# Kernel optimization log

Hardware: AMD Instinct MI355X
Metric: run time of the kernel (lower is better)

Reference implementation:

```python
import jax, jax.numpy as jnp
import numpy as np

HIDDEN = 1024
HEADS = 16
HEAD_DIM = HIDDEN // HEADS
B, S = 2, 2048


def setup_inputs() -> dict:
    key = jax.random.key(0)
    ks = jax.random.split(key, 11)
    std = 1.0 / np.sqrt(HIDDEN)
    return {
        "query": jax.random.normal(ks[0], (B, S, HIDDEN), dtype=jnp.float32),
        "key": jax.random.normal(ks[1], (B, S, HIDDEN), dtype=jnp.float32),
        "value": jax.random.normal(ks[2], (B, S, HIDDEN), dtype=jnp.float32),
        "Wq": jax.random.uniform(ks[3], (HIDDEN, HIDDEN), jnp.float32, -std, std),
        "bq": jax.random.uniform(ks[4], (HIDDEN,), jnp.float32, -std, std),
        "Wk": jax.random.uniform(ks[5], (HIDDEN, HIDDEN), jnp.float32, -std, std),
        "bk": jax.random.uniform(ks[6], (HIDDEN,), jnp.float32, -std, std),
        "Wv": jax.random.uniform(ks[7], (HIDDEN, HIDDEN), jnp.float32, -std, std),
        "bv": jax.random.uniform(ks[8], (HIDDEN,), jnp.float32, -std, std),
        "Wo": jax.random.uniform(ks[9], (HIDDEN, HIDDEN), jnp.float32, -std, std),
        "bo": jax.random.uniform(ks[10], (HIDDEN,), jnp.float32, -std, std),
    }


def reference(query, key, value, Wq, bq, Wk, bk, Wv, bv, Wo, bo):
    b = query.shape[0]
    scale = jnp.sqrt(jnp.float32(HEAD_DIM))
    # linear projections (torch Linear: x @ W.T + b), split into heads -> [b, h, s, d]
    def proj(x, W, bias):
        y = x @ W.T + bias
        return y.reshape(b, -1, HEADS, HEAD_DIM).transpose(0, 2, 1, 3)
    Q = proj(query, Wq, bq)
    K = proj(key, Wk, bk)
    V = proj(value, Wv, bv)
    scores = jnp.einsum("bhqd,bhkd->bhqk", Q, K) / scale
    attn = jax.nn.softmax(scores, axis=-1)
    ctx = jnp.einsum("bhqk,bhkd->bhqd", attn, V)
    ctx = ctx.transpose(0, 2, 1, 3).reshape(b, -1, HIDDEN)
    return ctx @ Wo.T + bo
```

## Files before the change

### kernel.cpp

```cpp
#include <hip/hip_runtime.h>

typedef __attribute__((ext_vector_type(8))) short short8;
typedef __attribute__((ext_vector_type(4))) float float4_t;
typedef __attribute__((ext_vector_type(4))) unsigned int uint4_t;
typedef __attribute__((ext_vector_type(2))) unsigned int uint2_t;
typedef unsigned short u16;

#define HIDDEN 1024
#define HDIM   64
#define SS     2048
#define TOK    4096
#define QSCALE 0.1803368801111137f

__device__ __forceinline__ unsigned int fbits(float f) {
  unsigned int x; __builtin_memcpy(&x, &f, 4); return x;
}
__device__ __forceinline__ u16 f2bf(float f) {
  return (u16)((fbits(f) + 0x8000u) >> 16);
}
__device__ __forceinline__ unsigned int pk2bf(float a, float b) {
  return __builtin_amdgcn_perm(fbits(b) + 0x8000u, fbits(a) + 0x8000u, 0x07060302);
}
__device__ __forceinline__ unsigned int pk2bf_t(float a, float b) {
  return __builtin_amdgcn_perm(fbits(b), fbits(a), 0x07060302);
}

__device__ __forceinline__ void gl_lds16(const u16* g, u16* l) {
  __builtin_amdgcn_global_load_lds(
      (const __attribute__((address_space(1))) unsigned int*)g,
      (__attribute__((address_space(3))) unsigned int*)l, 16, 0, 0);
}

__global__ __launch_bounds__(256) void convert_all(
    const float* __restrict__ w0, const float* __restrict__ w1,
    const float* __restrict__ w2, const float* __restrict__ w3,
    const float* __restrict__ x0, const float* __restrict__ x1,
    const float* __restrict__ x2, u16* __restrict__ Wall, u16* __restrict__ Xall) {
  int y = blockIdx.y;
  const float* src; u16* dst;
  if (y < 4) {
    if (blockIdx.x >= 512) return;
    src = y == 0 ? w0 : y == 1 ? w1 : y == 2 ? w2 : w3;
    dst = Wall + ((size_t)y << 20);
  } else {
    src = y == 4 ? x0 : y == 5 ? x1 : x2;
    dst = Xall + ((size_t)(y - 4) << 22);
  }
  int g = (blockIdx.x * 256 + threadIdx.x) * 8;
  float4_t a = *(const float4_t*)(src + g);
  float4_t b = *(const float4_t*)(src + g + 4);
  uint4_t o;
  o.x = pk2bf(a[0], a[1]); o.y = pk2bf(a[2], a[3]);
  o.z = pk2bf(b[0], b[1]); o.w = pk2bf(b[2], b[3]);
  *(uint4_t*)(dst + g) = o;
}

template<int MTILES, bool AXF32, bool OUTF32>
__device__ __forceinline__ void gemm_bt_body(
    const void* __restrict__ X, const u16* __restrict__ Wb,
    const float* __restrict__ bias, void* __restrict__ Y, int mode, float oscale,
    u16* sA, u16* sB, int row0, int col0) {
  const int tid  = threadIdx.x;
  const int wv   = tid >> 6, lane = tid & 63, quad = lane >> 4, ln = lane & 15;
  const int wm   = (wv >> 1) * (MTILES * 16), wn = (wv & 1) * 64;
  constexpr int AITERS = MTILES;

  float4_t acc[MTILES][4];
#pragma unroll
  for (int i = 0; i < MTILES; i++)
#pragma unroll
    for (int j = 0; j < 4; j++) acc[i][j] = (float4_t)0.0f;

  for (int kt = 0; kt < 16; ++kt) {
    const int k0 = kt * 64;
    short8 ax[AITERS];
    if (AXF32) {
#pragma unroll
      for (int i = 0; i < AITERS; i++) {
        int idx = i * 256 + tid, r = idx >> 3, c = idx & 7;
        const float* p = (const float*)X + (size_t)(row0 + r) * HIDDEN + k0 + c * 8;
        float4_t a = *(const float4_t*)p;
        float4_t b = *(const float4_t*)(p + 4);
        union { unsigned int u[4]; short8 s; } x;
        x.u[0] = pk2bf(a[0], a[1]); x.u[1] = pk2bf(a[2], a[3]);
        x.u[2] = pk2bf(b[0], b[1]); x.u[3] = pk2bf(b[2], b[3]);
        ax[i] = x.s;
      }
    }
    __syncthreads();
#pragma unroll
    for (int i = 0; i < 4; i++) {
      int idx = i * 256 + tid, r = idx >> 3, c = idx & 7;
      int gc = c ^ (r & 7);
      gl_lds16(Wb + (size_t)(col0 + r) * HIDDEN + k0 + gc * 8, sB + idx * 8);
    }
    if (AXF32) {
#pragma unroll
      for (int i = 0; i < AITERS; i++) {
        int idx = i * 256 + tid, r = idx >> 3, c = idx & 7;
        int pos = c ^ (r & 7);
        *(short8*)(sA + r * 64 + pos * 8) = ax[i];
      }
    } else {
#pragma unroll
      for (int i = 0; i < AITERS; i++) {
        int idx = i * 256 + tid, r = idx >> 3, c = idx & 7;
        int gc = c ^ (r & 7);
        gl_lds16((const u16*)X + (size_t)(row0 + r) * HIDDEN + k0 + gc * 8, sA + idx * 8);
      }
    }
    __syncthreads();

    short8 af[MTILES][2], bfr[4][2];
#pragma unroll
    for (int mt = 0; mt < MTILES; mt++)
#pragma unroll
      for (int kk = 0; kk < 2; kk++) {
        int r = wm + mt * 16 + ln;
        int ch = kk * 4 + quad;
        af[mt][kk] = *(const short8*)(sA + r * 64 + (ch ^ (r & 7)) * 8);
      }
#pragma unroll
    for (int nt = 0; nt < 4; nt++)
#pragma unroll
      for (int kk = 0; kk < 2; kk++) {
        int r = wn + nt * 16 + ln;
        int ch = kk * 4 + quad;
        bfr[nt][kk] = *(const short8*)(sB + r * 64 + (ch ^ (r & 7)) * 8);
      }
#pragma unroll
    for (int kk = 0; kk < 2; kk++)
#pragma unroll
      for (int mt = 0; mt < MTILES; mt++)
#pragma unroll
        for (int nt = 0; nt < 4; nt++)
          acc[mt][nt] = __builtin_amdgcn_mfma_f32_16x16x32_bf16(af[mt][kk], bfr[nt][kk], acc[mt][nt], 0, 0, 0);
  }

  float bcol[4];
#pragma unroll
  for (int nt = 0; nt < 4; nt++) bcol[nt] = bias[col0 + wn + nt * 16 + ln];
#pragma unroll
  for (int mt = 0; mt < MTILES; mt++)
#pragma unroll
    for (int nt = 0; nt < 4; nt++) {
      int n = col0 + wn + nt * 16 + ln;
#pragma unroll
      for (int r = 0; r < 4; r++) {
        int m = row0 + wm + mt * 16 + quad * 4 + r;
        float v = (acc[mt][nt][r] + bcol[nt]) * oscale;
        if (mode == 0) {
          if (OUTF32) ((float*)Y)[(size_t)m * HIDDEN + n] = v;
          else        ((u16*)Y)[(size_t)m * HIDDEN + n] = f2bf(v);
        } else {
          ((u16*)Y)[((size_t)(m >> 11) * HIDDEN + n) * SS + (m & 2047)] = f2bf(v);
        }
      }
    }
}

__global__ __launch_bounds__(256) void qkv_gemm_bf16(
    const u16* __restrict__ Xall, const u16* __restrict__ Wall,
    const float* __restrict__ bq, const float* __restrict__ bk, const float* __restrict__ bv,
    u16* __restrict__ Qp, u16* __restrict__ Kp, u16* __restrict__ Vt) {
  __shared__ u16 sA[128 * 64];
  __shared__ u16 sB[128 * 64];
  int z = blockIdx.z;
  const u16* X = Xall + ((size_t)z << 22);
  const u16* W = Wall + ((size_t)z << 20);
  const float* Bp = z == 0 ? bq : z == 1 ? bk : bv;
  u16* Y = z == 0 ? Qp : z == 1 ? Kp : Vt;
  int mode = (z == 2) ? 1 : 0;
  float sc = (z == 0) ? QSCALE : 1.0f;
  gemm_bt_body<4, false, false>(X, W, Bp, Y, mode, sc, sA, sB, blockIdx.y * 128, blockIdx.x * 128);
}

__global__ __launch_bounds__(256) void qkv_gemm_f32(
    const float* __restrict__ xq, const float* __restrict__ xk, const float* __restrict__ xv,
    const u16* __restrict__ Wall,
    const float* __restrict__ bq, const float* __restrict__ bk, const float* __restrict__ bv,
    u16* __restrict__ Qp, u16* __restrict__ Kp, u16* __restrict__ Vt) {
  __shared__ u16 sA[128 * 64];
  __shared__ u16 sB[128 * 64];
  int z = blockIdx.z;
  const float* X = z == 0 ? xq : z == 1 ? xk : xv;
  const u16* W = Wall + ((size_t)z << 20);
  const float* Bp = z == 0 ? bq : z == 1 ? bk : bv;
  u16* Y = z == 0 ? Qp : z == 1 ? Kp : Vt;
  int mode = (z == 2) ? 1 : 0;
  float sc = (z == 0) ? QSCALE : 1.0f;
  gemm_bt_body<4, true, false>(X, W, Bp, Y, mode, sc, sA, sB, blockIdx.y * 128, blockIdx.x * 128);
}

__global__ __launch_bounds__(256) void out_gemm(
    const u16* __restrict__ X, const u16* __restrict__ Wob,
    const float* __restrict__ bias, float* __restrict__ Y) {
  __shared__ u16 sA[64 * 64];
  __shared__ u16 sB[128 * 64];
  gemm_bt_body<2, false, true>(X, Wob, bias, Y, 0, 1.0f, sA, sB, blockIdx.y * 64, blockIdx.x * 128);
}

__global__ __launch_bounds__(256) void attn(
    const u16* __restrict__ Qp, const u16* __restrict__ Kp,
    const u16* __restrict__ Vt, u16* __restrict__ Ctx) {
  __shared__ u16 sK[128 * 64];
  __shared__ u16 sV[80 * 128];
  __shared__ u16 sP[4 * 32 * 64];
  const int tid  = threadIdx.x;
  const int wv   = tid >> 6, lane = tid & 63, quad = lane >> 4, ln = lane & 15;
  const int qt = blockIdx.x, h = blockIdx.y, b = blockIdx.z;
  const int row0 = qt * 128 + wv * 32;

  {
    int rr = 64 + (tid >> 4), cc = (tid & 15) * 8;
    short8 vv;
#pragma unroll
    for (int j = 0; j < 8; j++) vv[j] = (rr == 64) ? (short)0x3F80 : (short)0;
    *(short8*)(sV + rr * 128 + cc) = vv;
  }

  short8 qf[2][2];
#pragma unroll
  for (int j = 0; j < 2; j++)
#pragma unroll
    for (int kk = 0; kk < 2; kk++)
      qf[j][kk] = *(const short8*)(Qp + (size_t)(b * SS + row0 + j * 16 + ln) * HIDDEN
                                   + h * HDIM + kk * 32 + quad * 8);

  float4_t oacc[2][5];
#pragma unroll
  for (int j = 0; j < 2; j++)
#pragma unroll
    for (int t = 0; t < 5; t++) oacc[j][t] = (float4_t)0.f;

  u16* myP = sP + wv * 32 * 64;

  for (int kt = 0; kt < 16; ++kt) {
    __syncthreads();
#pragma unroll
    for (int p = 0; p < 4; p++) {
      int off = p * 256 + tid;
      { int r = off >> 3, c = off & 7;  int gc = c ^ (r & 7);
        gl_lds16(Kp + (size_t)(b * SS + kt * 128 + r) * HIDDEN + h * HDIM + gc * 8, sK + off * 8); }
      { int r = off >> 4, c = off & 15; int gc = c ^ (r & 15);
        gl_lds16(Vt + ((size_t)b * HIDDEN + h * HDIM + r) * SS + kt * 128 + gc * 8, sV + off * 8); }
    }
    __syncthreads();

#pragma unroll
    for (int half = 0; half < 2; half++) {
      float4_t st[4][2];
#pragma unroll
      for (int nt4 = 0; nt4 < 4; nt4++) {
        int nt = half * 4 + nt4;
#pragma unroll
        for (int j = 0; j < 2; j++) st[nt4][j] = (float4_t)0.f;
#pragma unroll
        for (int kk = 0; kk < 2; kk++) {
          int r = nt * 16 + ln;
          int ch = kk * 4 + quad;
          short8 kfr = *(const short8*)(sK + r * 64 + (ch ^ (r & 7)) * 8);
#pragma unroll
          for (int j = 0; j < 2; j++)
            st[nt4][j] = __builtin_amdgcn_mfma_f32_16x16x32_bf16(kfr, qf[j][kk], st[nt4][j], 0, 0, 0);
        }
      }

#pragma unroll
      for (int nt4 = 0; nt4 < 4; nt4++)
#pragma unroll
        for (int j = 0; j < 2; j++) {
          float p0 = __builtin_amdgcn_exp2f(fminf(st[nt4][j][0], 80.f));
          float p1 = __builtin_amdgcn_exp2f(fminf(st[nt4][j][1], 80.f));
          float p2 = __builtin_amdgcn_exp2f(fminf(st[nt4][j][2], 80.f));
          float p3 = __builtin_amdgcn_exp2f(fminf(st[nt4][j][3], 80.f));
          uint2_t w; w.x = pk2bf_t(p0, p1); w.y = pk2bf_t(p2, p3);
          int row = j * 16 + ln;
          int c2 = nt4 * 2 + (quad >> 1);
          int pos = c2 ^ (row & 7);
          *(uint2_t*)(myP + row * 64 + pos * 8 + (quad & 1) * 4) = w;
        }

#pragma unroll
      for (int ks = 0; ks < 2; ks++) {
        int CH = half * 8 + ks * 4 + quad;
        short8 vf[5];
#pragma unroll
        for (int dt = 0; dt < 5; dt++) {
          int d = dt * 16 + ln;
          vf[dt] = *(const short8*)(sV + d * 128 + ((CH ^ (d & 15))) * 8);
        }
#pragma unroll
        for (int j = 0; j < 2; j++) {
          int row = j * 16 + ln;
          int c2 = ks * 4 + quad;
          short8 pb = *(const short8*)(myP + row * 64 + (c2 ^ (row & 7)) * 8);
#pragma unroll
          for (int dt = 0; dt < 5; dt++)
            oacc[j][dt] = __builtin_amdgcn_mfma_f32_16x16x32_bf16(vf[dt], pb, oacc[j][dt], 0, 0, 0);
        }
      }
    }
  }

#pragma unroll
  for (int j = 0; j < 2; j++) {
    float inv = 1.0f / __shfl(oacc[j][4][0], ln, 64);
#pragma unroll
    for (int dt = 0; dt < 4; dt++) {
      uint2_t w;
      w.x = pk2bf(oacc[j][dt][0] * inv, oacc[j][dt][1] * inv);
      w.y = pk2bf(oacc[j][dt][2] * inv, oacc[j][dt][3] * inv);
      int row = j * 16 + ln;
      int ch = dt * 2 + (quad >> 1);
      int pos = ch ^ (row & 7);
      *(uint2_t*)(myP + row * 64 + pos * 8 + (quad & 1) * 4) = w;
    }
  }
#pragma unroll
  for (int jr = 0; jr < 2; jr++)
#pragma unroll
    for (int jc = 0; jc < 2; jc++) {
      int q = lane >> 2;
      int row = jr * 16 + q;
      int c = jc * 4 + (lane & 3);
      int pos = c ^ (row & 7);
      short8 o8 = *(const short8*)(myP + row * 64 + pos * 8);
      *(short8*)(Ctx + (size_t)(b * SS + row0 + row) * HIDDEN + h * HDIM + c * 8) = o8;
    }
}

extern "C" void kernel_launch(void* const* d_in, const int* in_sizes, int n_in,
                              void* d_out, int out_size, void* d_ws, size_t ws_size,
                              hipStream_t stream) {
  const float* q  = (const float*)d_in[0];
  const float* k  = (const float*)d_in[1];
  const float* v  = (const float*)d_in[2];
  const float* Wq = (const float*)d_in[3];
  const float* bq = (const float*)d_in[4];
  const float* Wk = (const float*)d_in[5];
  const float* bk = (const float*)d_in[6];
  const float* Wv = (const float*)d_in[7];
  const float* bv = (const float*)d_in[8];
  const float* Wo = (const float*)d_in[9];
  const float* bo = (const float*)d_in[10];

  u16* Qp   = (u16*)d_ws;
  u16* Kp   = Qp + (size_t)TOK * HIDDEN;
  u16* Vt   = Kp + (size_t)TOK * HIDDEN;
  u16* Wall = Vt + (size_t)TOK * HIDDEN;
  u16* Xall = Wall + (4u << 20);
  u16* Cx   = Qp;
  bool useX = ws_size >= (size_t)56 * 1024 * 1024;

  dim3 blk(256);
  if (useX) {
    hipLaunchKernelGGL(convert_all, dim3(2048, 7), blk, 0, stream,
                       Wq, Wk, Wv, Wo, q, k, v, Wall, Xall);
    hipLaunchKernelGGL(qkv_gemm_bf16, dim3(8, 32, 3), blk, 0, stream,
                       Xall, Wall, bq, bk, bv, Qp, Kp, Vt);
  } else {
    hipLaunchKernelGGL(convert_all, dim3(512, 4), blk, 0, stream,
                       Wq, Wk, Wv, Wo, q, k, v, Wall, Wall);
    hipLaunchKernelGGL(qkv_gemm_f32, dim3(8, 32, 3), blk, 0, stream,
                       q, k, v, Wall, bq, bk, bv, Qp, Kp, Vt);
  }
  hipLaunchKernelGGL(attn, dim3(16, 16, 2), blk, 0, stream, Qp, Kp, Vt, Cx);
  hipLaunchKernelGGL(out_gemm, dim3(8, 64, 1), blk, 0, stream,
                     Cx, Wall + (3u << 20), bo, (float*)d_out);
}
```

Baseline: 236.0 us.

## Rewrite attention with 32x32 MFMA, register-resident P, and double-buffered K/V

The attention kernel moves from 16x16x32 to 32x32x16 bf16 MFMA, with each wave covering 64 query rows. Softmax probabilities are repacked in registers via permlane32_swap, so the LDS round trip for P goes away. The row sum is accumulated in registers, which drops the extra ones-row MFMA tile. K/V tiles are double-buffered so loading the next tile overlaps compute, the grid becomes a flat 256 blocks (one per CU), and launch bounds are set to one block per SM. The trade-off is higher register pressure and lower occupancy, plus a grid that relies on a fixed 256-CU mapping.

```diff
diff --git a/kernel.cpp b/kernel.cpp
--- a/kernel.cpp
+++ b/kernel.cpp
@@ -2,6 +2,7 @@
 
 typedef __attribute__((ext_vector_type(8))) short short8;
 typedef __attribute__((ext_vector_type(4))) float float4_t;
+typedef __attribute__((ext_vector_type(16))) float f32x16;
 typedef __attribute__((ext_vector_type(4))) unsigned int uint4_t;
 typedef __attribute__((ext_vector_type(2))) unsigned int uint2_t;
 typedef unsigned short u16;
@@ -200,134 +201,135 @@
   gemm_bt_body<2, false, true>(X, Wob, bias, Y, 0, 1.0f, sA, sB, blockIdx.y * 64, blockIdx.x * 128);
 }
 
-__global__ __launch_bounds__(256) void attn(
+__global__ __launch_bounds__(256, 1) void attn(
     const u16* __restrict__ Qp, const u16* __restrict__ Kp,
     const u16* __restrict__ Vt, u16* __restrict__ Ctx) {
-  __shared__ u16 sK[128 * 64];
-  __shared__ u16 sV[80 * 128];
-  __shared__ u16 sP[4 * 32 * 64];
+  __shared__ u16 sK[2][128 * 64];
+  __shared__ u16 sV[2][64 * 128];
   const int tid  = threadIdx.x;
-  const int wv   = tid >> 6, lane = tid & 63, quad = lane >> 4, ln = lane & 15;
-  const int qt = blockIdx.x, h = blockIdx.y, b = blockIdx.z;
-  const int row0 = qt * 128 + wv * 32;
-
-  {
-    int rr = 64 + (tid >> 4), cc = (tid & 15) * 8;
-    short8 vv;
-#pragma unroll
-    for (int j = 0; j < 8; j++) vv[j] = (rr == 64) ? (short)0x3F80 : (short)0;
-    *(short8*)(sV + rr * 128 + cc) = vv;
-  }
-
-  short8 qf[2][2];
-#pragma unroll
-  for (int j = 0; j < 2; j++)
-#pragma unroll
-    for (int kk = 0; kk < 2; kk++)
-      qf[j][kk] = *(const short8*)(Qp + (size_t)(b * SS + row0 + j * 16 + ln) * HIDDEN
-                                   + h * HDIM + kk * 32 + quad * 8);
-
-  float4_t oacc[2][5];
-#pragma unroll
-  for (int j = 0; j < 2; j++)
-#pragma unroll
-    for (int t = 0; t < 5; t++) oacc[j][t] = (float4_t)0.f;
-
-  u16* myP = sP + wv * 32 * 64;
-
-  for (int kt = 0; kt < 16; ++kt) {
-    __syncthreads();
-#pragma unroll
-    for (int p = 0; p < 4; p++) {
+  const int wv   = tid >> 6, lane = tid & 63;
+  const int l5   = lane >> 5, ln = lane & 31;
+  const int f = blockIdx.x;
+  const int qt = f >> 5, g = f & 31, h = g >> 1, b = g & 1;
+  const int row0w = qt * 256 + wv * 64;
+
+  short8 qf[2][4];
+#pragma unroll
+  for (int qg = 0; qg < 2; ++qg)
+#pragma unroll
+    for (int kk = 0; kk < 4; ++kk)
+      qf[qg][kk] = *(const short8*)(Qp + (size_t)(b * SS + row0w + qg * 32 + ln) * HIDDEN
+                                    + h * HDIM + kk * 16 + l5 * 8);
+
+  f32x16 oacc[2][2];
+#pragma unroll
+  for (int qg = 0; qg < 2; ++qg)
+#pragma unroll
+    for (int dg = 0; dg < 2; ++dg) oacc[qg][dg] = (f32x16)0.0f;
+  float dsum[2] = {0.f, 0.f};
+
+  auto stage = [&](int buf, int kt) {
+#pragma unroll
+    for (int p = 0; p < 4; ++p) {
       int off = p * 256 + tid;
       { int r = off >> 3, c = off & 7;  int gc = c ^ (r & 7);
-        gl_lds16(Kp + (size_t)(b * SS + kt * 128 + r) * HIDDEN + h * HDIM + gc * 8, sK + off * 8); }
+        gl_lds16(Kp + (size_t)(b * SS + kt * 128 + r) * HIDDEN + h * HDIM + gc * 8,
+                 &sK[buf][0] + off * 8); }
       { int r = off >> 4, c = off & 15; int gc = c ^ (r & 15);
-        gl_lds16(Vt + ((size_t)b * HIDDEN + h * HDIM + r) * SS + kt * 128 + gc * 8, sV + off * 8); }
+        gl_lds16(Vt + ((size_t)b * HIDDEN + h * HDIM + r) * SS + kt * 128 + gc * 8,
+                 &sV[buf][0] + off * 8); }
+    }
+  };
+
+  stage(0, 0);
+  __syncthreads();
+
+  for (int kt = 0; kt < 16; ++kt) {
+    const int cur = kt & 1;
+    if (kt < 15) stage(cur ^ 1, kt + 1);
+    const u16* K_ = &sK[cur][0];
+    const u16* V_ = &sV[cur][0];
+
+#pragma unroll
+    for (int kgg = 0; kgg < 4; ++kgg) {
+      f32x16 st[2];
+      st[0] = (f32x16)0.0f; st[1] = (f32x16)0.0f;
+#pragma unroll
+      for (int kk = 0; kk < 4; ++kk) {
+        int r = kgg * 32 + ln;
+        int ch = kk * 2 + l5;
+        short8 kf = *(const short8*)(K_ + r * 64 + ((ch ^ (r & 7))) * 8);
+        st[0] = __builtin_amdgcn_mfma_f32_32x32x16_bf16(kf, qf[0][kk], st[0], 0, 0, 0);
+        st[1] = __builtin_amdgcn_mfma_f32_32x32x16_bf16(kf, qf[1][kk], st[1], 0, 0, 0);
+      }
+
+      union PF { unsigned int u[4]; short8 s; };
+      PF pfr[2][2];
+#pragma unroll
+      for (int qg = 0; qg < 2; ++qg) {
+        float p[16];
+#pragma unroll
+        for (int r = 0; r < 16; ++r)
+          p[r] = __builtin_amdgcn_exp2f(fminf(st[qg][r], 80.f));
+        dsum[qg] += (((p[0] + p[1]) + (p[2] + p[3])) + ((p[4] + p[5]) + (p[6] + p[7])))
+                  + (((p[8] + p[9]) + (p[10] + p[11])) + ((p[12] + p[13]) + (p[14] + p[15])));
+        unsigned int pk[8];
+#pragma unroll
+        for (int i = 0; i < 8; ++i) pk[i] = pk2bf_t(p[2 * i], p[2 * i + 1]);
+        uint2_t r02 = __builtin_amdgcn_permlane32_swap(pk[0], pk[2], false, false);
+        uint2_t r13 = __builtin_amdgcn_permlane32_swap(pk[1], pk[3], false, false);
+        uint2_t r46 = __builtin_amdgcn_permlane32_swap(pk[4], pk[6], false, false);
+        uint2_t r57 = __builtin_amdgcn_permlane32_swap(pk[5], pk[7], false, false);
+        pfr[qg][0].u[0] = r02.x; pfr[qg][0].u[1] = r13.x;
+        pfr[qg][0].u[2] = r02.y; pfr[qg][0].u[3] = r13.y;
+        pfr[qg][1].u[0] = r46.x; pfr[qg][1].u[1] = r57.x;
+        pfr[qg][1].u[2] = r46.y; pfr[qg][1].u[3] = r57.y;
+      }
+
+#pragma unroll
+      for (int ks = 0; ks < 2; ++ks) {
+        int ch = (kgg * 2 + ks) * 2 + l5;
+#pragma unroll
+        for (int dg = 0; dg < 2; ++dg) {
+          int r = dg * 32 + ln;
+          short8 vf = *(const short8*)(V_ + r * 128 + ((ch ^ (r & 15))) * 8);
+          oacc[0][dg] = __builtin_amdgcn_mfma_f32_32x32x16_bf16(vf, pfr[0][ks].s, oacc[0][dg], 0, 0, 0);
+          oacc[1][dg] = __builtin_amdgcn_mfma_f32_32x32x16_bf16(vf, pfr[1][ks].s, oacc[1][dg], 0, 0, 0);
+        }
+      }
     }
     __syncthreads();
-
-#pragma unroll
-    for (int half = 0; half < 2; half++) {
-      float4_t st[4][2];
-#pragma unroll
-      for (int nt4 = 0; nt4 < 4; nt4++) {
-        int nt = half * 4 + nt4;
-#pragma unroll
-        for (int j = 0; j < 2; j++) st[nt4][j] = (float4_t)0.f;
-#pragma unroll
-        for (int kk = 0; kk < 2; kk++) {
-          int r = nt * 16 + ln;
-          int ch = kk * 4 + quad;
-          short8 kfr = *(const short8*)(sK + r * 64 + (ch ^ (r & 7)) * 8);
-#pragma unroll
-          for (int j = 0; j < 2; j++)
-            st[nt4][j] = __builtin_amdgcn_mfma_f32_16x16x32_bf16(kfr, qf[j][kk], st[nt4][j], 0, 0, 0);
-        }
-      }
-
-#pragma unroll
-      for (int nt4 = 0; nt4 < 4; nt4++)
-#pragma unroll
-        for (int j = 0; j < 2; j++) {
-          float p0 = __builtin_amdgcn_exp2f(fminf(st[nt4][j][0], 80.f));
-          float p1 = __builtin_amdgcn_exp2f(fminf(st[nt4][j][1], 80.f));
-          float p2 = __builtin_amdgcn_exp2f(fminf(st[nt4][j][2], 80.f));
-          float p3 = __builtin_amdgcn_exp2f(fminf(st[nt4][j][3], 80.f));
-          uint2_t w; w.x = pk2bf_t(p0, p1); w.y = pk2bf_t(p2, p3);
-          int row = j * 16 + ln;
-          int c2 = nt4 * 2 + (quad >> 1);
-          int pos = c2 ^ (row & 7);
-          *(uint2_t*)(myP + row * 64 + pos * 8 + (quad & 1) * 4) = w;
-        }
-
-#pragma unroll
-      for (int ks = 0; ks < 2; ks++) {
-        int CH = half * 8 + ks * 4 + quad;
-        short8 vf[5];
-#pragma unroll
-        for (int dt = 0; dt < 5; dt++) {
-          int d = dt * 16 + ln;
-          vf[dt] = *(const short8*)(sV + d * 128 + ((CH ^ (d & 15))) * 8);
-        }
-#pragma unroll
-        for (int j = 0; j < 2; j++) {
-          int row = j * 16 + ln;
-          int c2 = ks * 4 + quad;
-          short8 pb = *(const short8*)(myP + row * 64 + (c2 ^ (row & 7)) * 8);
-#pragma unroll
-          for (int dt = 0; dt < 5; dt++)
-            oacc[j][dt] = __builtin_amdgcn_mfma_f32_16x16x32_bf16(vf[dt], pb, oacc[j][dt], 0, 0, 0);
-        }
-      }
-    }
-  }
-
-#pragma unroll
-  for (int j = 0; j < 2; j++) {
-    float inv = 1.0f / __shfl(oacc[j][4][0], ln, 64);
-#pragma unroll
-    for (int dt = 0; dt < 4; dt++) {
-      uint2_t w;
-      w.x = pk2bf(oacc[j][dt][0] * inv, oacc[j][dt][1] * inv);
-      w.y = pk2bf(oacc[j][dt][2] * inv, oacc[j][dt][3] * inv);
-      int row = j * 16 + ln;
-      int ch = dt * 2 + (quad >> 1);
-      int pos = ch ^ (row & 7);
-      *(uint2_t*)(myP + row * 64 + pos * 8 + (quad & 1) * 4) = w;
-    }
-  }
-#pragma unroll
-  for (int jr = 0; jr < 2; jr++)
-#pragma unroll
-    for (int jc = 0; jc < 2; jc++) {
-      int q = lane >> 2;
-      int row = jr * 16 + q;
-      int c = jc * 4 + (lane & 3);
-      int pos = c ^ (row & 7);
-      short8 o8 = *(const short8*)(myP + row * 64 + pos * 8);
-      *(short8*)(Ctx + (size_t)(b * SS + row0 + row) * HIDDEN + h * HDIM + c * 8) = o8;
-    }
+  }
+
+  float inv[2];
+#pragma unroll
+  for (int qg = 0; qg < 2; ++qg) {
+    float s = dsum[qg] + __shfl_xor(dsum[qg], 32, 64);
+    inv[qg] = 1.0f / s;
+  }
+
+  u16* ep = ((u16*)sK) + wv * 4096;
+#pragma unroll
+  for (int qg = 0; qg < 2; ++qg) {
+    int row = qg * 32 + ln;
+#pragma unroll
+    for (int dg = 0; dg < 2; ++dg)
+#pragma unroll
+      for (int i = 0; i < 4; ++i) {
+        uint2_t w;
+        w.x = pk2bf(oacc[qg][dg][4 * i] * inv[qg],     oacc[qg][dg][4 * i + 1] * inv[qg]);
+        w.y = pk2bf(oacc[qg][dg][4 * i + 2] * inv[qg], oacc[qg][dg][4 * i + 3] * inv[qg]);
+        int c = dg * 4 + i;
+        *(uint2_t*)(ep + row * 64 + ((c ^ (row & 7))) * 8 + l5 * 4) = w;
+      }
+  }
+#pragma unroll
+  for (int ps = 0; ps < 8; ++ps) {
+    int r = ps * 8 + (lane >> 3);
+    int c = lane & 7;
+    short8 o8 = *(const short8*)(ep + r * 64 + ((c ^ (r & 7))) * 8);
+    *(short8*)(Ctx + (size_t)(b * SS + row0w + r) * HIDDEN + h * HDIM + c * 8) = o8;
+  }
 }
 
 extern "C" void kernel_launch(void* const* d_in, const int* in_sizes, int n_in,
@@ -365,7 +367,7 @@
     hipLaunchKernelGGL(qkv_gemm_f32, dim3(8, 32, 3), blk, 0, stream,
                        q, k, v, Wall, bq, bk, bv, Qp, Kp, Vt);
   }
-  hipLaunchKernelGGL(attn, dim3(16, 16, 2), blk, 0, stream, Qp, Kp, Vt, Cx);
+  hipLaunchKernelGGL(attn, dim3(256), blk, 0, stream, Qp, Kp, Vt, Cx);
   hipLaunchKernelGGL(out_gemm, dim3(8, 64, 1), blk, 0, stream,
                      Cx, Wall + (3u << 20), bo, (float*)d_out);
 }
```

Result: slower. 243.3 us (+3.1%).
